# Kernel tuning notes

Hardware: AMD Instinct MI355X
Metric: run time of the kernel (lower is better)

The kernel has to match this reference:

```python
import jax, jax.numpy as jnp
import numpy as np
from jax import lax

NH = 8          # num_heads
DK = 256        # depth_k
DV = 256        # depth_v
DKH = DK // NH  # per-head key depth
DVH = DV // NH  # per-head value depth


def setup_inputs() -> dict:
    key = jax.random.key(0)
    k1, k2, k3 = jax.random.split(key, 3)
    B, C, H, W = 8, 256, 32, 32
    x = jax.random.normal(k1, (B, C, H, W), dtype=jnp.float32)
    # fan-in scaled init (glorot-like) to keep conv outputs / attention logits sane
    conv_w = jax.random.normal(k2, (3, 3, 256, 256), dtype=jnp.float32) / np.sqrt(3 * 3 * 256)
    conv_b = jnp.zeros((256,), dtype=jnp.float32)
    attn_w = jax.random.normal(k3, (1, 1, 256, 768), dtype=jnp.float32) / np.sqrt(256)
    attn_b = jnp.zeros((768,), dtype=jnp.float32)
    return {"x": x, "conv_w": conv_w, "conv_b": conv_b, "attn_w": attn_w, "attn_b": attn_b}


def _conv2d_same(x, w, b):
    # x: (B,C,H,W), w: (kh,kw,Cin,Cout) -> (B,Cout,H,W)
    y = lax.conv_general_dilated(x, w, window_strides=(1, 1), padding="SAME",
                                 dimension_numbers=("NCHW", "HWIO", "NCHW"))
    return y + b[None, :, None, None]


def reference(x, conv_w, conv_b, attn_w, attn_b):
    B, C, H, W = x.shape
    HW = H * W

    # parallel conv branch: channels_out - depth_v = 256 output channels
    conv_out = _conv2d_same(x, conv_w, conv_b)

    # 1x1 conv producing K, Q, V (split order matches tf.split([dk, dk, dv]))
    kqv = _conv2d_same(x, attn_w, attn_b)
    k = kqv[:, :DK]
    q = kqv[:, DK:2 * DK] * (DKH ** -0.5)
    v = kqv[:, 2 * DK:]

    # (B, Nh, d, HW) per-head flattening; token axis = HW
    def heads(t, d):
        return t.reshape(B, NH, d, HW)

    qh, kh, vh = heads(q, DKH), heads(k, DKH), heads(v, DVH)

    # logits: (B, Nh, HW, HW)
    logits = jnp.einsum("bhdn,bhdm->bhnm", qh, kh)
    weights = jax.nn.softmax(logits, axis=-1)
    # attn: (B, Nh, HW, dvh)
    attn = jnp.einsum("bhnm,bhdm->bhnd", weights, vh)

    # combine heads: (B,Nh,H,W,dvh) -> channel order (nh, dvh) -> (B, depth_v, H, W)
    attn_out = attn.reshape(B, NH, H, W, DVH).transpose(0, 1, 4, 2, 3).reshape(B, DV, H, W)

    return jnp.concatenate([conv_out, attn_out], axis=1)
```

## Files before the change

kernel.cpp:

```cpp
#include <hip/hip_runtime.h>


typedef __attribute__((ext_vector_type(8))) short short8;
typedef __attribute__((ext_vector_type(4))) float f32x4;
typedef unsigned short u16;

#define QSCALE 0.25503487629898483f

__device__ inline u16 f2bf(float f) {
  unsigned u = __builtin_bit_cast(unsigned, f);
  return (u16)((u + 0x7FFFu + ((u >> 16) & 1u)) >> 16);
}
__device__ inline unsigned pack2bf(float a, float b) {
  return (unsigned)f2bf(a) | ((unsigned)f2bf(b) << 16);
}
__device__ inline unsigned packP(float a, float b) {
  unsigned au = __builtin_bit_cast(unsigned, a) + 0x8000u;
  unsigned bu = __builtin_bit_cast(unsigned, b) + 0x8000u;
  return __builtin_amdgcn_perm(bu, au, 0x07060302u);
}
__device__ inline float hmax4(f32x4 v) {
  return fmaxf(fmaxf(v[0], v[1]), fmaxf(v[2], v[3]));
}
__device__ inline float hsum4(f32x4 v) { return (v[0] + v[1]) + (v[2] + v[3]); }

__global__ __launch_bounds__(256) void prep_kernel(const float* __restrict__ x,
                                                   const float* __restrict__ cw,
                                                   const float* __restrict__ aw,
                                                   u16* __restrict__ xT,
                                                   u16* __restrict__ WcT,
                                                   u16* __restrict__ WaT) {
  __shared__ float T[64][65];
  int bid = blockIdx.x, tid = threadIdx.x;

  if (bid < 128) {
    int b = bid >> 4, n0 = (bid & 15) * 64;
#pragma unroll
    for (int rep = 0; rep < 2; ++rep) {
      int flat = rep * 256 + tid;
      int n = flat & 63, cg = flat >> 6;
#pragma unroll
      for (int q = 0; q < 4; ++q) {
        short8 pk;
#pragma unroll
        for (int j = 0; j < 8; ++j)
          pk[j] =
              (short)f2bf(x[(b * 256 + cg * 32 + q * 8 + j) * 1024 + n0 + n]);
        *(short8*)&xT[(b * 1024 + n0 + n) * 256 + cg * 32 + q * 8] = pk;
      }
    }
    return;
  }

  int tt = bid - 128;
  int chunk = tt >> 4, t = tt & 15;
  int ci0 = (t & 3) * 64, r0 = (t >> 2) * 64;
  bool isconv = chunk < 9;
  float scale = (chunk == 10) ? QSCALE : 1.0f;

#pragma unroll
  for (int rep = 0; rep < 16; ++rep) {
    int flat = rep * 256 + tid;
    int i = flat >> 6, j = flat & 63;
    T[i][j] = isconv ? cw[(chunk * 256 + ci0 + i) * 256 + r0 + j]
                     : aw[(ci0 + i) * 768 + (chunk - 9) * 256 + r0 + j];
  }
  __syncthreads();
#pragma unroll
  for (int rep = 0; rep < 4; ++rep) {
    int flat = rep * 256 + tid;
    int jj = flat >> 4, qq = flat & 15;
    float v0 = T[qq * 4 + 0][jj] * scale;
    float v1 = T[qq * 4 + 1][jj] * scale;
    float v2 = T[qq * 4 + 2][jj] * scale;
    float v3 = T[qq * 4 + 3][jj] * scale;
    uint2 pk = {pack2bf(v0, v1), pack2bf(v2, v3)};
    if (isconv)
      *(uint2*)&WcT[(chunk * 256 + r0 + jj) * 256 + ci0 + qq * 4] = pk;
    else
      *(uint2*)&WaT[((chunk - 9) * 256 + r0 + jj) * 256 + ci0 + qq * 4] = pk;
  }
}

__global__ __launch_bounds__(256) void kqv_kernel(const u16* __restrict__ xT,
                                                  const u16* __restrict__ WaT,
                                                  const float* __restrict__ ab,
                                                  u16* __restrict__ kT,
                                                  u16* __restrict__ qT,
                                                  u16* __restrict__ vB) {
  __shared__ __align__(16) u16 Tt[64 * 136];
  int bid = blockIdx.x;
  int b = bid & 7, idx = bid >> 3;
  int ot = idx >> 4, nt = idx & 15;
  int tid = threadIdx.x, wave = tid >> 6, lane = tid & 63;
  int ln = lane & 15, g = lane >> 4;
  int o0 = ot * 128 + (wave & 1) * 64;
  int n0 = nt * 64 + (wave >> 1) * 32;
  const u16* xb = xT + b * 1024 * 256;
  f32x4 acc[4][2];
#pragma unroll
  for (int i = 0; i < 4; ++i)
#pragma unroll
    for (int j = 0; j < 2; ++j) acc[i][j] = (f32x4){0.f, 0.f, 0.f, 0.f};

#pragma unroll
  for (int c0 = 0; c0 < 256; c0 += 32) {
    int ko = c0 + g * 8;
    short8 a0 = *(const short8*)&WaT[(o0 + ln) * 256 + ko];
    short8 a1 = *(const short8*)&WaT[(o0 + 16 + ln) * 256 + ko];
    short8 a2 = *(const short8*)&WaT[(o0 + 32 + ln) * 256 + ko];
    short8 a3 = *(const short8*)&WaT[(o0 + 48 + ln) * 256 + ko];
    short8 b0 = *(const short8*)&xb[(n0 + ln) * 256 + ko];
    short8 b1 = *(const short8*)&xb[(n0 + 16 + ln) * 256 + ko];
    acc[0][0] = __builtin_amdgcn_mfma_f32_16x16x32_bf16(a0, b0, acc[0][0], 0, 0, 0);
    acc[0][1] = __builtin_amdgcn_mfma_f32_16x16x32_bf16(a0, b1, acc[0][1], 0, 0, 0);
    acc[1][0] = __builtin_amdgcn_mfma_f32_16x16x32_bf16(a1, b0, acc[1][0], 0, 0, 0);
    acc[1][1] = __builtin_amdgcn_mfma_f32_16x16x32_bf16(a1, b1, acc[1][1], 0, 0, 0);
    acc[2][0] = __builtin_amdgcn_mfma_f32_16x16x32_bf16(a2, b0, acc[2][0], 0, 0, 0);
    acc[2][1] = __builtin_amdgcn_mfma_f32_16x16x32_bf16(a2, b1, acc[2][1], 0, 0, 0);
    acc[3][0] = __builtin_amdgcn_mfma_f32_16x16x32_bf16(a3, b0, acc[3][0], 0, 0, 0);
    acc[3][1] = __builtin_amdgcn_mfma_f32_16x16x32_bf16(a3, b1, acc[3][1], 0, 0, 0);
  }

  if (ot >= 4) {
#pragma unroll
    for (int it = 0; it < 4; ++it)
#pragma unroll
      for (int r = 0; r < 4; ++r) {
        int o = o0 + it * 16 + g * 4 + r;
        float bias = ab[o];
#pragma unroll
        for (int jt = 0; jt < 2; ++jt) {
          int n = n0 + jt * 16 + ln;
          vB[(b * 256 + (o - 512)) * 1024 + n] = f2bf(acc[it][jt][r] + bias);
        }
      }
    return;
  }

  bool isQ = (ot >= 2);
  float bs = isQ ? QSCALE : 1.0f;
  int olb = (wave & 1) * 64;
  int nlb = (wave >> 1) * 32;
#pragma unroll
  for (int it = 0; it < 4; ++it)
#pragma unroll
    for (int jt = 0; jt < 2; ++jt) {
      int ol = olb + it * 16 + g * 4;
      int nl = nlb + jt * 16 + ln;
      int og = ot * 128 + ol;
      float v0 = acc[it][jt][0] + ab[og + 0] * bs;
      float v1 = acc[it][jt][1] + ab[og + 1] * bs;
      float v2 = acc[it][jt][2] + ab[og + 2] * bs;
      float v3 = acc[it][jt][3] + ab[og + 3] * bs;
      uint2 pk = {pack2bf(v0, v1), pack2bf(v2, v3)};
      *(uint2*)&Tt[nl * 136 + ol] = pk;
    }
  __syncthreads();
  u16* dst = isQ ? qT : kT;
#pragma unroll
  for (int rep = 0; rep < 4; ++rep) {
    int flat = rep * 256 + tid;
    int o8 = flat & 15, nl = flat >> 4;
    short8 v = *(const short8*)&Tt[nl * 136 + o8 * 8];
    int og256 = (ot & 1) * 128 + o8 * 8;
    int hh = og256 >> 5, d0 = og256 & 31;
    int ng = nt * 64 + nl;
    *(short8*)&dst[((b * 8 + hh) * 1024 + ng) * 32 + d0] = v;
  }
}

__global__ __launch_bounds__(256, 2) void conv_attn_kernel(
    const u16* __restrict__ xT, const u16* __restrict__ WcT,
    const float* __restrict__ cb, const u16* __restrict__ kT,
    const u16* __restrict__ qT, const u16* __restrict__ vB,
    float* __restrict__ out) {
  __shared__ __align__(16) unsigned char smem[32768];

  int bid = blockIdx.x;
  int b = bid & 7;
  int sub = bid >> 3;
  int trip = sub / 3;
  int rem = sub - trip * 3;
  int tid = threadIdx.x;
  int wave = tid >> 6, lane = tid & 63;
  int ln = lane & 15, g = lane >> 4;

  if (rem == 2) {
    u16* Xc = (u16*)smem;
    int hp = trip >> 1, coh = trip & 1;
    int h0 = hp * 2;
    int co0 = coh * 128 + wave * 32;

    f32x4 acc[2][4];
#pragma unroll
    for (int i = 0; i < 2; ++i)
#pragma unroll
      for (int j = 0; j < 4; ++j) acc[i][j] = (f32x4){0.f, 0.f, 0.f, 0.f};

    {
      int rp = tid >> 6, rest = tid & 63;
      int which = rest >> 5, cp = rest & 31;
      *(unsigned*)&Xc[(rp * 34 + which * 33) * 72 + cp * 2] = 0u;
    }

    for (int c0 = 0; c0 < 256; c0 += 64) {
      __syncthreads();
#pragma unroll
      for (int rep = 0; rep < 4; ++rep) {
        int flat = rep * 256 + tid;
        int cg = flat & 7, w = (flat >> 3) & 31, rp = flat >> 8;
        int row = h0 - 1 + rp;
        short8 v = {0, 0, 0, 0, 0, 0, 0, 0};
        if ((unsigned)row < 32u)
          v = *(const short8*)&xT[(b * 1024 + row * 32 + w) * 256 + c0 + cg * 8];
        int rowS = rp * 34 + w + 1;
        *(short8*)&Xc[rowS * 72 + ((cg ^ (rowS & 7)) * 8)] = v;
      }
      __syncthreads();
#pragma unroll
      for (int ks = 0; ks < 2; ++ks) {
        int ko = c0 + ks * 32 + g * 8;
        int slot = ks * 4 + g;
#pragma unroll
        for (int r = 0; r < 3; ++r)
#pragma unroll
          for (int s = 0; s < 3; ++s) {
            int tap = r * 3 + s;
            short8 a0 = *(const short8*)&WcT[(tap * 256 + co0 + ln) * 256 + ko];
            short8 a1 =
                *(const short8*)&WcT[(tap * 256 + co0 + 16 + ln) * 256 + ko];
#pragma unroll
            for (int jt = 0; jt < 4; ++jt) {
              int rowp = ((jt >> 1) + r) * 34 + (jt & 1) * 16 + ln + s;
              short8 bf =
                  *(const short8*)&Xc[rowp * 72 + ((slot ^ (rowp & 7)) * 8)];
              acc[0][jt] = __builtin_amdgcn_mfma_f32_16x16x32_bf16(
                  a0, bf, acc[0][jt], 0, 0, 0);
              acc[1][jt] = __builtin_amdgcn_mfma_f32_16x16x32_bf16(
                  a1, bf, acc[1][jt], 0, 0, 0);
            }
          }
      }
    }

#pragma unroll
    for (int it = 0; it < 2; ++it)
#pragma unroll
      for (int r4 = 0; r4 < 4; ++r4) {
        int co = co0 + it * 16 + g * 4 + r4;
        float bias = cb[co];
#pragma unroll
        for (int jt = 0; jt < 4; ++jt) {
          int h = h0 + (jt >> 1), w = (jt & 1) * 16 + ln;
          out[((b * 512 + co) * 32 + h) * 32 + w] = acc[it][jt][r4] + bias;
        }
      }
    return;
  }

  u16* kvb = (u16*)smem;
  u16* ps = (u16*)(smem + 16384);
  int idx = trip * 2 + rem;
  int h = idx >> 3, qt = idx & 7;
  int nw = qt * 128 + wave * 32;

  const u16* kb = kT + (b * 8 + h) * (1024 * 32);
  const u16* qb = qT + (b * 8 + h) * (1024 * 32);
  const u16* vb = vB + (b * 256 + h * 32) * 1024;

  short8 qf0 = *(const short8*)&qb[(nw + ln) * 32 + g * 8];
  short8 qf1 = *(const short8*)&qb[(nw + 16 + ln) * 32 + g * 8];

  int sr = tid >> 2, ss = tid & 3;
  int dvr = tid >> 3, vs = tid & 7;
  const u16* ksrc = kb + sr * 32 + ss * 8;
  const u16* vsrc = vb + dvr * 1024 + vs * 8;
  int kdsw = sr * 32 + ((ss ^ ((sr + (sr >> 2)) & 3)) * 8);
  int vdsw = 2048 + dvr * 64 + ((vs ^ (dvr & 7)) * 8);

  int skl = (ln + (ln >> 2)) & 3;
  int svl = ln & 7;
  int kfo = ln * 32 + ((g ^ skl) * 8);

  f32x4 o00 = {0.f, 0.f, 0.f, 0.f}, o01 = o00, o10 = o00, o11 = o00;
  float mx0 = -1e30f, mx1 = -1e30f, l0 = 0.f, l1 = 0.f;
  u16* pw0 = ps + wave * 2048;
  u16* pw1 = pw0 + 1024;

  short8 kp = *(const short8*)ksrc;
  short8 vp = *(const short8*)vsrc;
  *(short8*)&kvb[kdsw] = kp;
  *(short8*)&kvb[vdsw] = vp;
  __syncthreads();
  kp = *(const short8*)(ksrc + 2048);
  vp = *(const short8*)(vsrc + 64);

  for (int mt = 0; mt < 16; ++mt) {
    u16* bc = kvb + (mt & 1) * 4096;
    if (mt < 15) {
      u16* bn = kvb + ((mt + 1) & 1) * 4096;
      *(short8*)&bn[kdsw] = kp;
      *(short8*)&bn[vdsw] = vp;
    }
    if (mt < 14) {
      kp = *(const short8*)(ksrc + (mt + 2) * 2048);
      vp = *(const short8*)(vsrc + (mt + 2) * 64);
    }

    short8 ka0 = *(const short8*)&bc[0 * 512 + kfo];
    short8 ka1 = *(const short8*)&bc[1 * 512 + kfo];
    short8 ka2 = *(const short8*)&bc[2 * 512 + kfo];
    short8 ka3 = *(const short8*)&bc[3 * 512 + kfo];
    f32x4 z = {0.f, 0.f, 0.f, 0.f};
    f32x4 s0[4], s1[4];
    __builtin_amdgcn_s_setprio(1);
    s0[0] = __builtin_amdgcn_mfma_f32_16x16x32_bf16(ka0, qf0, z, 0, 0, 0);
    s1[0] = __builtin_amdgcn_mfma_f32_16x16x32_bf16(ka0, qf1, z, 0, 0, 0);
    s0[1] = __builtin_amdgcn_mfma_f32_16x16x32_bf16(ka1, qf0, z, 0, 0, 0);
    s1[1] = __builtin_amdgcn_mfma_f32_16x16x32_bf16(ka1, qf1, z, 0, 0, 0);
    s0[2] = __builtin_amdgcn_mfma_f32_16x16x32_bf16(ka2, qf0, z, 0, 0, 0);
    s1[2] = __builtin_amdgcn_mfma_f32_16x16x32_bf16(ka2, qf1, z, 0, 0, 0);
    s0[3] = __builtin_amdgcn_mfma_f32_16x16x32_bf16(ka3, qf0, z, 0, 0, 0);
    s1[3] = __builtin_amdgcn_mfma_f32_16x16x32_bf16(ka3, qf1, z, 0, 0, 0);
    __builtin_amdgcn_s_setprio(0);

    short8 va00 = *(const short8*)&bc[2048 + ln * 64 + ((g ^ svl) * 8)];
    short8 va01 = *(const short8*)&bc[2048 + (16 + ln) * 64 + ((g ^ svl) * 8)];
    short8 va10 = *(const short8*)&bc[2048 + ln * 64 + (((4 + g) ^ svl) * 8)];
    short8 va11 =
        *(const short8*)&bc[2048 + (16 + ln) * 64 + (((4 + g) ^ svl) * 8)];

    float tmax0 = fmaxf(fmaxf(hmax4(s0[0]), hmax4(s0[1])),
                        fmaxf(hmax4(s0[2]), hmax4(s0[3])));
    float tmax1 = fmaxf(fmaxf(hmax4(s1[0]), hmax4(s1[1])),
                        fmaxf(hmax4(s1[2]), hmax4(s1[3])));
    tmax0 = fmaxf(tmax0, __shfl_xor(tmax0, 16));
    tmax0 = fmaxf(tmax0, __shfl_xor(tmax0, 32));
    tmax1 = fmaxf(tmax1, __shfl_xor(tmax1, 16));
    tmax1 = fmaxf(tmax1, __shfl_xor(tmax1, 32));

    if (!__all(fmaxf(tmax0 - mx0, tmax1 - mx1) <= 8.0f)) {
      float nm0 = fmaxf(mx0, tmax0), nm1 = fmaxf(mx1, tmax1);
      float sc0 = __builtin_amdgcn_exp2f(mx0 - nm0);
      float sc1 = __builtin_amdgcn_exp2f(mx1 - nm1);
#pragma unroll
      for (int r = 0; r < 4; ++r) {
        o00[r] *= sc0; o01[r] *= sc0;
        o10[r] *= sc1; o11[r] *= sc1;
      }
      l0 *= sc0; l1 *= sc1;
      mx0 = nm0; mx1 = nm1;
    }

#pragma unroll
    for (int kt = 0; kt < 4; ++kt)
#pragma unroll
      for (int r = 0; r < 4; ++r) {
        s0[kt][r] = __builtin_amdgcn_exp2f(s0[kt][r] - mx0);
        s1[kt][r] = __builtin_amdgcn_exp2f(s1[kt][r] - mx1);
      }
    float ts0 = (hsum4(s0[0]) + hsum4(s0[1])) + (hsum4(s0[2]) + hsum4(s0[3]));
    float ts1 = (hsum4(s1[0]) + hsum4(s1[1])) + (hsum4(s1[2]) + hsum4(s1[3]));
    ts0 += __shfl_xor(ts0, 16); ts0 += __shfl_xor(ts0, 32);
    ts1 += __shfl_xor(ts1, 16); ts1 += __shfl_xor(ts1, 32);
    l0 += ts0; l1 += ts1;

#pragma unroll
    for (int kt = 0; kt < 4; ++kt) {
      int po = ln * 64 + (((kt * 2 + (g >> 1)) ^ svl) * 8) + (g & 1) * 4;
      uint2 w0 = {packP(s0[kt][0], s0[kt][1]), packP(s0[kt][2], s0[kt][3])};
      *(uint2*)&pw0[po] = w0;
      uint2 w1 = {packP(s1[kt][0], s1[kt][1]), packP(s1[kt][2], s1[kt][3])};
      *(uint2*)&pw1[po] = w1;
    }
    short8 pb00 = *(const short8*)&pw0[ln * 64 + ((g ^ svl) * 8)];
    short8 pb01 = *(const short8*)&pw0[ln * 64 + (((4 + g) ^ svl) * 8)];
    short8 pb10 = *(const short8*)&pw1[ln * 64 + ((g ^ svl) * 8)];
    short8 pb11 = *(const short8*)&pw1[ln * 64 + (((4 + g) ^ svl) * 8)];

    __builtin_amdgcn_s_setprio(1);
    o00 = __builtin_amdgcn_mfma_f32_16x16x32_bf16(va00, pb00, o00, 0, 0, 0);
    o01 = __builtin_amdgcn_mfma_f32_16x16x32_bf16(va01, pb00, o01, 0, 0, 0);
    o00 = __builtin_amdgcn_mfma_f32_16x16x32_bf16(va10, pb01, o00, 0, 0, 0);
    o01 = __builtin_amdgcn_mfma_f32_16x16x32_bf16(va11, pb01, o01, 0, 0, 0);
    o10 = __builtin_amdgcn_mfma_f32_16x16x32_bf16(va00, pb10, o10, 0, 0, 0);
    o11 = __builtin_amdgcn_mfma_f32_16x16x32_bf16(va01, pb10, o11, 0, 0, 0);
    o10 = __builtin_amdgcn_mfma_f32_16x16x32_bf16(va10, pb11, o10, 0, 0, 0);
    o11 = __builtin_amdgcn_mfma_f32_16x16x32_bf16(va11, pb11, o11, 0, 0, 0);
    __builtin_amdgcn_s_setprio(0);

    __syncthreads();
  }

  float rl0 = 1.f / l0, rl1 = 1.f / l1;
  float* obase = out + (b * 512 + 256 + h * 32) * 1024;
  float* ob0 = obase + nw + ln;
  float* ob1 = obase + nw + 16 + ln;
#pragma unroll
  for (int r = 0; r < 4; ++r) {
    int dv0 = g * 4 + r;
    ob0[dv0 * 1024] = o00[r] * rl0;
    ob0[(16 + dv0) * 1024] = o01[r] * rl0;
    ob1[dv0 * 1024] = o10[r] * rl1;
    ob1[(16 + dv0) * 1024] = o11[r] * rl1;
  }
}

extern "C" void kernel_launch(void* const* d_in, const int* in_sizes, int n_in,
                              void* d_out, int out_size, void* d_ws,
                              size_t ws_size, hipStream_t stream) {
  const float* x  = (const float*)d_in[0];
  const float* cw = (const float*)d_in[1];
  const float* cb = (const float*)d_in[2];
  const float* aw = (const float*)d_in[3];
  const float* ab = (const float*)d_in[4];
  float* out = (float*)d_out;

  char* ws = (char*)d_ws;
  u16* vB  = (u16*)ws;
  u16* kT  = (u16*)(ws + 4194304);
  u16* qT  = (u16*)(ws + 8388608);
  u16* xT  = (u16*)(ws + 12582912);
  u16* WcT = (u16*)(ws + 16777216);
  u16* WaT = (u16*)(ws + 17956864);

  prep_kernel<<<320, 256, 0, stream>>>(x, cw, aw, xT, WcT, WaT);
  kqv_kernel<<<768, 256, 0, stream>>>(xT, WaT, ab, kT, qT, vB);
  conv_attn_kernel<<<768, 256, 0, stream>>>(xT, WcT, cb, kT, qT, vB, out);
}
```

Baseline: 64.53 us.

## Switch attention to 32x32x16 MFMA and pass P through registers instead of LDS

Rewrites the attention inner loop to use 32x32x16 bf16 MFMAs, so each wave handles 32 queries as one tile with one running max and sum per lane. The softmax probabilities are now repacked into the B-operand layout with cross-half lane shuffles rather than a round trip through shared memory. The XOR-swizzled K/V layouts are replaced by padded row strides, and shared memory shrinks from 32 KB to about 19 KB. This removes the LDS traffic for P and reduces reduction shuffles, at the cost of more lane shuffles and register pressure from the 16-wide accumulators.

```diff
diff --git a/kernel.cpp b/kernel.cpp
--- a/kernel.cpp
+++ b/kernel.cpp
@@ -3,6 +3,7 @@
 
 typedef __attribute__((ext_vector_type(8))) short short8;
 typedef __attribute__((ext_vector_type(4))) float f32x4;
+typedef __attribute__((ext_vector_type(16))) float f32x16;
 typedef unsigned short u16;
 
 #define QSCALE 0.25503487629898483f
@@ -19,10 +20,6 @@
   unsigned bu = __builtin_bit_cast(unsigned, b) + 0x8000u;
   return __builtin_amdgcn_perm(bu, au, 0x07060302u);
 }
-__device__ inline float hmax4(f32x4 v) {
-  return fmaxf(fmaxf(v[0], v[1]), fmaxf(v[2], v[3]));
-}
-__device__ inline float hsum4(f32x4 v) { return (v[0] + v[1]) + (v[2] + v[3]); }
 
 __global__ __launch_bounds__(256) void prep_kernel(const float* __restrict__ x,
                                                    const float* __restrict__ cw,
@@ -175,7 +172,7 @@
     const float* __restrict__ cb, const u16* __restrict__ kT,
     const u16* __restrict__ qT, const u16* __restrict__ vB,
     float* __restrict__ out) {
-  __shared__ __align__(16) unsigned char smem[32768];
+  __shared__ __align__(16) unsigned char smem[19584];
 
   int bid = blockIdx.x;
   int b = bid & 7;
@@ -184,9 +181,9 @@
   int rem = sub - trip * 3;
   int tid = threadIdx.x;
   int wave = tid >> 6, lane = tid & 63;
-  int ln = lane & 15, g = lane >> 4;
 
   if (rem == 2) {
+    int ln = lane & 15, g = lane >> 4;
     u16* Xc = (u16*)smem;
     int hp = trip >> 1, coh = trip & 1;
     int h0 = hp * 2;
@@ -260,150 +257,130 @@
   }
 
   u16* kvb = (u16*)smem;
-  u16* ps = (u16*)(smem + 16384);
   int idx = trip * 2 + rem;
   int h = idx >> 3, qt = idx & 7;
   int nw = qt * 128 + wave * 32;
+  int lq = lane & 31, hi = lane >> 5;
 
   const u16* kb = kT + (b * 8 + h) * (1024 * 32);
   const u16* qb = qT + (b * 8 + h) * (1024 * 32);
   const u16* vb = vB + (b * 256 + h * 32) * 1024;
 
-  short8 qf0 = *(const short8*)&qb[(nw + ln) * 32 + g * 8];
-  short8 qf1 = *(const short8*)&qb[(nw + 16 + ln) * 32 + g * 8];
+  short8 qf0 = *(const short8*)&qb[(nw + lq) * 32 + hi * 8];
+  short8 qf1 = *(const short8*)&qb[(nw + lq) * 32 + 16 + hi * 8];
 
   int sr = tid >> 2, ss = tid & 3;
   int dvr = tid >> 3, vs = tid & 7;
   const u16* ksrc = kb + sr * 32 + ss * 8;
   const u16* vsrc = vb + dvr * 1024 + vs * 8;
-  int kdsw = sr * 32 + ((ss ^ ((sr + (sr >> 2)) & 3)) * 8);
-  int vdsw = 2048 + dvr * 64 + ((vs ^ (dvr & 7)) * 8);
-
-  int skl = (ln + (ln >> 2)) & 3;
-  int svl = ln & 7;
-  int kfo = ln * 32 + ((g ^ skl) * 8);
-
-  f32x4 o00 = {0.f, 0.f, 0.f, 0.f}, o01 = o00, o10 = o00, o11 = o00;
-  float mx0 = -1e30f, mx1 = -1e30f, l0 = 0.f, l1 = 0.f;
-  u16* pw0 = ps + wave * 2048;
-  u16* pw1 = pw0 + 1024;
+  int kdst = sr * 40 + ss * 8;
+  int vdst = 2560 + dvr * 72 + vs * 8;
+
+  int kr0 = lq * 40;
+  int kr1 = (32 + lq) * 40;
+  int vr = 2560 + lq * 72;
+
+  f32x16 o0 = {};
+  float mx = -1e30f, l = 0.f;
 
   short8 kp = *(const short8*)ksrc;
   short8 vp = *(const short8*)vsrc;
-  *(short8*)&kvb[kdsw] = kp;
-  *(short8*)&kvb[vdsw] = vp;
+  *(short8*)&kvb[kdst] = kp;
+  *(short8*)&kvb[vdst] = vp;
   __syncthreads();
   kp = *(const short8*)(ksrc + 2048);
   vp = *(const short8*)(vsrc + 64);
 
   for (int mt = 0; mt < 16; ++mt) {
-    u16* bc = kvb + (mt & 1) * 4096;
+    u16* bc = kvb + (mt & 1) * 4864;
     if (mt < 15) {
-      u16* bn = kvb + ((mt + 1) & 1) * 4096;
-      *(short8*)&bn[kdsw] = kp;
-      *(short8*)&bn[vdsw] = vp;
+      u16* bn = kvb + ((mt + 1) & 1) * 4864;
+      *(short8*)&bn[kdst] = kp;
+      *(short8*)&bn[vdst] = vp;
     }
     if (mt < 14) {
       kp = *(const short8*)(ksrc + (mt + 2) * 2048);
       vp = *(const short8*)(vsrc + (mt + 2) * 64);
     }
 
-    short8 ka0 = *(const short8*)&bc[0 * 512 + kfo];
-    short8 ka1 = *(const short8*)&bc[1 * 512 + kfo];
-    short8 ka2 = *(const short8*)&bc[2 * 512 + kfo];
-    short8 ka3 = *(const short8*)&bc[3 * 512 + kfo];
-    f32x4 z = {0.f, 0.f, 0.f, 0.f};
-    f32x4 s0[4], s1[4];
+    short8 ka00 = *(const short8*)&bc[kr0 + hi * 8];
+    short8 ka01 = *(const short8*)&bc[kr0 + 16 + hi * 8];
+    short8 ka10 = *(const short8*)&bc[kr1 + hi * 8];
+    short8 ka11 = *(const short8*)&bc[kr1 + 16 + hi * 8];
+    f32x16 s0t = {}, s1t = {};
     __builtin_amdgcn_s_setprio(1);
-    s0[0] = __builtin_amdgcn_mfma_f32_16x16x32_bf16(ka0, qf0, z, 0, 0, 0);
-    s1[0] = __builtin_amdgcn_mfma_f32_16x16x32_bf16(ka0, qf1, z, 0, 0, 0);
-    s0[1] = __builtin_amdgcn_mfma_f32_16x16x32_bf16(ka1, qf0, z, 0, 0, 0);
-    s1[1] = __builtin_amdgcn_mfma_f32_16x16x32_bf16(ka1, qf1, z, 0, 0, 0);
-    s0[2] = __builtin_amdgcn_mfma_f32_16x16x32_bf16(ka2, qf0, z, 0, 0, 0);
-    s1[2] = __builtin_amdgcn_mfma_f32_16x16x32_bf16(ka2, qf1, z, 0, 0, 0);
-    s0[3] = __builtin_amdgcn_mfma_f32_16x16x32_bf16(ka3, qf0, z, 0, 0, 0);
-    s1[3] = __builtin_amdgcn_mfma_f32_16x16x32_bf16(ka3, qf1, z, 0, 0, 0);
+    s0t = __builtin_amdgcn_mfma_f32_32x32x16_bf16(ka00, qf0, s0t, 0, 0, 0);
+    s0t = __builtin_amdgcn_mfma_f32_32x32x16_bf16(ka01, qf1, s0t, 0, 0, 0);
+    s1t = __builtin_amdgcn_mfma_f32_32x32x16_bf16(ka10, qf0, s1t, 0, 0, 0);
+    s1t = __builtin_amdgcn_mfma_f32_32x32x16_bf16(ka11, qf1, s1t, 0, 0, 0);
     __builtin_amdgcn_s_setprio(0);
 
-    short8 va00 = *(const short8*)&bc[2048 + ln * 64 + ((g ^ svl) * 8)];
-    short8 va01 = *(const short8*)&bc[2048 + (16 + ln) * 64 + ((g ^ svl) * 8)];
-    short8 va10 = *(const short8*)&bc[2048 + ln * 64 + (((4 + g) ^ svl) * 8)];
-    short8 va11 =
-        *(const short8*)&bc[2048 + (16 + ln) * 64 + (((4 + g) ^ svl) * 8)];
-
-    float tmax0 = fmaxf(fmaxf(hmax4(s0[0]), hmax4(s0[1])),
-                        fmaxf(hmax4(s0[2]), hmax4(s0[3])));
-    float tmax1 = fmaxf(fmaxf(hmax4(s1[0]), hmax4(s1[1])),
-                        fmaxf(hmax4(s1[2]), hmax4(s1[3])));
-    tmax0 = fmaxf(tmax0, __shfl_xor(tmax0, 16));
-    tmax0 = fmaxf(tmax0, __shfl_xor(tmax0, 32));
-    tmax1 = fmaxf(tmax1, __shfl_xor(tmax1, 16));
-    tmax1 = fmaxf(tmax1, __shfl_xor(tmax1, 32));
-
-    if (!__all(fmaxf(tmax0 - mx0, tmax1 - mx1) <= 8.0f)) {
-      float nm0 = fmaxf(mx0, tmax0), nm1 = fmaxf(mx1, tmax1);
-      float sc0 = __builtin_amdgcn_exp2f(mx0 - nm0);
-      float sc1 = __builtin_amdgcn_exp2f(mx1 - nm1);
-#pragma unroll
-      for (int r = 0; r < 4; ++r) {
-        o00[r] *= sc0; o01[r] *= sc0;
-        o10[r] *= sc1; o11[r] *= sc1;
-      }
-      l0 *= sc0; l1 *= sc1;
-      mx0 = nm0; mx1 = nm1;
-    }
-
-#pragma unroll
-    for (int kt = 0; kt < 4; ++kt)
-#pragma unroll
-      for (int r = 0; r < 4; ++r) {
-        s0[kt][r] = __builtin_amdgcn_exp2f(s0[kt][r] - mx0);
-        s1[kt][r] = __builtin_amdgcn_exp2f(s1[kt][r] - mx1);
-      }
-    float ts0 = (hsum4(s0[0]) + hsum4(s0[1])) + (hsum4(s0[2]) + hsum4(s0[3]));
-    float ts1 = (hsum4(s1[0]) + hsum4(s1[1])) + (hsum4(s1[2]) + hsum4(s1[3]));
-    ts0 += __shfl_xor(ts0, 16); ts0 += __shfl_xor(ts0, 32);
-    ts1 += __shfl_xor(ts1, 16); ts1 += __shfl_xor(ts1, 32);
-    l0 += ts0; l1 += ts1;
-
-#pragma unroll
-    for (int kt = 0; kt < 4; ++kt) {
-      int po = ln * 64 + (((kt * 2 + (g >> 1)) ^ svl) * 8) + (g & 1) * 4;
-      uint2 w0 = {packP(s0[kt][0], s0[kt][1]), packP(s0[kt][2], s0[kt][3])};
-      *(uint2*)&pw0[po] = w0;
-      uint2 w1 = {packP(s1[kt][0], s1[kt][1]), packP(s1[kt][2], s1[kt][3])};
-      *(uint2*)&pw1[po] = w1;
-    }
-    short8 pb00 = *(const short8*)&pw0[ln * 64 + ((g ^ svl) * 8)];
-    short8 pb01 = *(const short8*)&pw0[ln * 64 + (((4 + g) ^ svl) * 8)];
-    short8 pb10 = *(const short8*)&pw1[ln * 64 + ((g ^ svl) * 8)];
-    short8 pb11 = *(const short8*)&pw1[ln * 64 + (((4 + g) ^ svl) * 8)];
+    short8 vf0 = *(const short8*)&bc[vr + hi * 8];
+    short8 vf1 = *(const short8*)&bc[vr + 16 + hi * 8];
+    short8 vf2 = *(const short8*)&bc[vr + 32 + hi * 8];
+    short8 vf3 = *(const short8*)&bc[vr + 48 + hi * 8];
+
+    float tmax = s0t[0];
+#pragma unroll
+    for (int r = 1; r < 16; ++r) tmax = fmaxf(tmax, s0t[r]);
+#pragma unroll
+    for (int r = 0; r < 16; ++r) tmax = fmaxf(tmax, s1t[r]);
+    tmax = fmaxf(tmax, __shfl_xor(tmax, 32));
+
+    if (!__all(tmax - mx <= 8.0f)) {
+      float nm = fmaxf(mx, tmax);
+      float sc = __builtin_amdgcn_exp2f(mx - nm);
+#pragma unroll
+      for (int r = 0; r < 16; ++r) o0[r] *= sc;
+      l *= sc;
+      mx = nm;
+    }
+
+#pragma unroll
+    for (int r = 0; r < 16; ++r) {
+      s0t[r] = __builtin_amdgcn_exp2f(s0t[r] - mx);
+      s1t[r] = __builtin_amdgcn_exp2f(s1t[r] - mx);
+    }
+    float ts = 0.f;
+#pragma unroll
+    for (int r = 0; r < 16; ++r) ts += s0t[r] + s1t[r];
+    ts += __shfl_xor(ts, 32);
+    l += ts;
 
     __builtin_amdgcn_s_setprio(1);
-    o00 = __builtin_amdgcn_mfma_f32_16x16x32_bf16(va00, pb00, o00, 0, 0, 0);
-    o01 = __builtin_amdgcn_mfma_f32_16x16x32_bf16(va01, pb00, o01, 0, 0, 0);
-    o00 = __builtin_amdgcn_mfma_f32_16x16x32_bf16(va10, pb01, o00, 0, 0, 0);
-    o01 = __builtin_amdgcn_mfma_f32_16x16x32_bf16(va11, pb01, o01, 0, 0, 0);
-    o10 = __builtin_amdgcn_mfma_f32_16x16x32_bf16(va00, pb10, o10, 0, 0, 0);
-    o11 = __builtin_amdgcn_mfma_f32_16x16x32_bf16(va01, pb10, o11, 0, 0, 0);
-    o10 = __builtin_amdgcn_mfma_f32_16x16x32_bf16(va10, pb11, o10, 0, 0, 0);
-    o11 = __builtin_amdgcn_mfma_f32_16x16x32_bf16(va11, pb11, o11, 0, 0, 0);
+#define PV_CHUNK(SV, CB, VF)                                                  \
+  {                                                                           \
+    unsigned A0 = packP(SV[(CB) + 0], SV[(CB) + 1]);                          \
+    unsigned A1 = packP(SV[(CB) + 2], SV[(CB) + 3]);                          \
+    unsigned B0 = packP(SV[(CB) + 4], SV[(CB) + 5]);                          \
+    unsigned B1 = packP(SV[(CB) + 6], SV[(CB) + 7]);                          \
+    unsigned sm0 = hi ? A0 : B0, sm1 = hi ? A1 : B1;                          \
+    unsigned r0_ = (unsigned)__shfl_xor((int)sm0, 32);                        \
+    unsigned r1_ = (unsigned)__shfl_xor((int)sm1, 32);                        \
+    uint4 fw;                                                                 \
+    fw.x = hi ? r0_ : A0;                                                     \
+    fw.y = hi ? r1_ : A1;                                                     \
+    fw.z = hi ? B0 : r0_;                                                     \
+    fw.w = hi ? B1 : r1_;                                                     \
+    short8 pf = __builtin_bit_cast(short8, fw);                               \
+    o0 = __builtin_amdgcn_mfma_f32_32x32x16_bf16(VF, pf, o0, 0, 0, 0);        \
+  }
+    PV_CHUNK(s0t, 0, vf0)
+    PV_CHUNK(s0t, 8, vf1)
+    PV_CHUNK(s1t, 0, vf2)
+    PV_CHUNK(s1t, 8, vf3)
+#undef PV_CHUNK
     __builtin_amdgcn_s_setprio(0);
 
     __syncthreads();
   }
 
-  float rl0 = 1.f / l0, rl1 = 1.f / l1;
-  float* obase = out + (b * 512 + 256 + h * 32) * 1024;
-  float* ob0 = obase + nw + ln;
-  float* ob1 = obase + nw + 16 + ln;
-#pragma unroll
-  for (int r = 0; r < 4; ++r) {
-    int dv0 = g * 4 + r;
-    ob0[dv0 * 1024] = o00[r] * rl0;
-    ob0[(16 + dv0) * 1024] = o01[r] * rl0;
-    ob1[dv0 * 1024] = o10[r] * rl1;
-    ob1[(16 + dv0) * 1024] = o11[r] * rl1;
+  float rl = 1.f / l;
+  float* ob = out + (b * 512 + 256 + h * 32) * 1024 + nw + lq;
+#pragma unroll
+  for (int r = 0; r < 16; ++r) {
+    int dv = (r & 3) + 8 * (r >> 2) + 4 * hi;
+    ob[dv * 1024] = o0[r] * rl;
   }
 }
 
```

Result: no change. 65.39 us (+1.3%).
